# Performance work log

Measured on AMD Instinct MI355X. Metric: run time of the kernel, lower is better.

## Reference

```python
import jax, jax.numpy as jnp
import numpy as np

M, B, T, DIN, H, E, NEMB = 6, 128, 32, 64, 512, 512, 32


def setup_inputs() -> dict:
    key = jax.random.key(0)
    ks = jax.random.split(key, 6)
    return {
        "state_btD": jax.random.normal(ks[0], (B, T, M * DIN), dtype=jnp.float32),
        "emb_ids": jax.random.randint(ks[1], (B,), 0, NEMB),
        # stacked per-modality, per-embodiment adapter params (all modalities share dims)
        "W1": 0.02 * jax.random.normal(ks[2], (M, NEMB, DIN, H), dtype=jnp.float32),
        "b1": jnp.zeros((M, NEMB, H), dtype=jnp.float32),
        "W2": 0.02 * jax.random.normal(ks[3], (M, NEMB, H, E), dtype=jnp.float32),
        "b2": jnp.zeros((M, NEMB, E), dtype=jnp.float32),
        "type_embed": 0.02 * jax.random.normal(ks[4], (M, E), dtype=jnp.float32),
    }


def reference(state_btD, emb_ids, W1, b1, W2, b2, type_embed):
    Bb, Tt, _ = state_btD.shape
    # slices are contiguous equal-size chunks -> (B, T, M, DIN)
    x = state_btD.reshape(Bb, Tt, M, DIN)
    # layer1: per-sample gathered weights W1[:, emb_ids] -> (M, B, DIN, H)
    h = jax.nn.relu(
        jnp.einsum('btmi,mbih->btmh', x, W1[:, emb_ids])
        + b1[:, emb_ids].transpose(1, 0, 2)[:, None]  # (B,1,M,H)
    )
    # layer2 + type embed
    z = (
        jnp.einsum('btmh,mbho->btmo', h, W2[:, emb_ids])
        + b2[:, emb_ids].transpose(1, 0, 2)[:, None]
        + type_embed[None, None]  # (1,1,M,E)
    )
    # torch.cat(tokens, dim=1): modality-major along the token axis -> (B, M*T, E)
    return z.transpose(0, 2, 1, 3).reshape(Bb, M * Tt, E)
```

## Files before the change

kernel.cpp:

```cpp
#include <hip/hip_runtime.h>

#define MM   6
#define BB   128
#define TT   32
#define DIN  64
#define HH   512
#define EE   512
#define NEMB 32
#define XP   72
#define HP   520
#define TRS  36

typedef __attribute__((ext_vector_type(8))) short bf16x8;
typedef __attribute__((ext_vector_type(4))) float f32x4;

static __device__ __forceinline__ unsigned short f2bf(float f) {
    unsigned int u = __float_as_uint(f);
    u += 0x7FFFu + ((u >> 16) & 1u);
    return (unsigned short)(u >> 16);
}
static __device__ __forceinline__ float bf2f(unsigned short h) {
    return __uint_as_float(((unsigned int)h) << 16);
}

__global__ void order_k(const int* __restrict__ emb_ids, int* __restrict__ ent) {
    __shared__ int cnt_s[NEMB], psum_s[NEMB], slot_s[BB], id_s[BB];
    int t = threadIdx.x;
    if (t < NEMB) cnt_s[t] = 0;
    __syncthreads();
    if (t < BB) { int id = emb_ids[t]; id_s[t] = id; slot_s[t] = atomicAdd(&cnt_s[id], 1); }
    __syncthreads();
    if (t == 0) { int r = 0; for (int i = 0; i < NEMB; ++i) { psum_s[i] = r; r += cnt_s[i]; } }
    __syncthreads();
    if (t < BB) {
        int id = id_s[t], sl = slot_s[t], base = psum_s[id] * MM, c = cnt_s[id];
        for (int mm = 0; mm < MM; ++mm) ent[base + mm * c + sl] = (t << 3) | mm;
    }
}

__global__ __launch_bounds__(256, 2) void tok_mfma4(
    const float* __restrict__ state,
    const int*   __restrict__ ent,
    const float* __restrict__ W1,
    const float* __restrict__ b1,
    const float* __restrict__ W2,
    const float* __restrict__ b2,
    const float* __restrict__ te,
    const int*   __restrict__ emb_ids,
    float* __restrict__ out)
{
    __shared__ __align__(16) unsigned char regA[10240];
    __shared__ __align__(16) unsigned short h_hi[TT][HP];
    __shared__ __align__(16) unsigned short h_lo[TT][HP];

    const int bid = blockIdx.x;
    const int s   = (bid & 7) * 96 + (bid >> 3);
    const int e   = ent[s];
    const int b   = e >> 3;
    const int m   = e & 7;
    const int id  = emb_ids[b];

    const int tid  = threadIdx.x;
    const int lane = tid & 63;
    const int w    = tid >> 6;
    const int lr   = lane & 15;
    const int lg   = lane >> 4;

    const float* W1p = W1 + (size_t)(m * NEMB + id) * DIN * HH;
    const float* b1p = b1 + (size_t)(m * NEMB + id) * HH;
    const float* W2p = W2 + (size_t)(m * NEMB + id) * HH * EE;
    const float* b2p = b2 + (size_t)(m * NEMB + id) * EE;
    const float* tep = te + m * EE;
    const float* xg  = state + (size_t)b * TT * (MM * DIN) + m * DIN;

    unsigned short (*x_hi)[XP] = (unsigned short(*)[XP])regA;
    unsigned short (*x_lo)[XP] = (unsigned short(*)[XP])(regA + 4608);

    #pragma unroll
    for (int kq = 0; kq < 2; ++kq) {
        int f  = kq * 256 + tid;
        int t  = f >> 4;
        int i4 = f & 15;
        float4 v = *reinterpret_cast<const float4*>(xg + (size_t)t * (MM * DIN) + i4 * 4);
        ushort4 hi, lo;
        hi.x = f2bf(v.x); lo.x = f2bf(v.x - bf2f(hi.x));
        hi.y = f2bf(v.y); lo.y = f2bf(v.y - bf2f(hi.y));
        hi.z = f2bf(v.z); lo.z = f2bf(v.z - bf2f(hi.z));
        hi.w = f2bf(v.w); lo.w = f2bf(v.w - bf2f(hi.w));
        *reinterpret_cast<ushort4*>(&x_hi[t][i4 * 4]) = hi;
        *reinterpret_cast<ushort4*>(&x_lo[t][i4 * 4]) = lo;
    }
    __syncthreads();

    bf16x8 xa_h[2][2], xa_l[2][2];
    #pragma unroll
    for (int rt = 0; rt < 2; ++rt)
        #pragma unroll
        for (int kk = 0; kk < 2; ++kk) {
            xa_h[rt][kk] = *reinterpret_cast<const bf16x8*>(&x_hi[rt * 16 + lr][kk * 32 + lg * 8]);
            xa_l[rt][kk] = *reinterpret_cast<const bf16x8*>(&x_lo[rt * 16 + lr][kk * 32 + lg * 8]);
        }

    #pragma unroll
    for (int j = 0; j < 8; ++j) {
        const int n = w * 128 + j * 16 + lr;
        float bv = b1p[n];
        f32x4 a0 = {bv, bv, bv, bv};
        f32x4 a1 = {bv, bv, bv, bv};
        #pragma unroll
        for (int kk = 0; kk < 2; ++kk) {
            const float* wp = W1p + (size_t)(kk * 32 + lg * 8) * HH + n;
            bf16x8 bh, bl;
            #pragma unroll
            for (int i = 0; i < 8; ++i) {
                float wv = wp[(size_t)i * HH];
                unsigned short h_ = f2bf(wv);
                bh[i] = (short)h_;
                bl[i] = (short)f2bf(wv - bf2f(h_));
            }
            a0 = __builtin_amdgcn_mfma_f32_16x16x32_bf16(xa_h[0][kk], bh, a0, 0, 0, 0);
            a0 = __builtin_amdgcn_mfma_f32_16x16x32_bf16(xa_h[0][kk], bl, a0, 0, 0, 0);
            a0 = __builtin_amdgcn_mfma_f32_16x16x32_bf16(xa_l[0][kk], bh, a0, 0, 0, 0);
            a1 = __builtin_amdgcn_mfma_f32_16x16x32_bf16(xa_h[1][kk], bh, a1, 0, 0, 0);
            a1 = __builtin_amdgcn_mfma_f32_16x16x32_bf16(xa_h[1][kk], bl, a1, 0, 0, 0);
            a1 = __builtin_amdgcn_mfma_f32_16x16x32_bf16(xa_l[1][kk], bh, a1, 0, 0, 0);
        }
        #pragma unroll
        for (int r = 0; r < 4; ++r) {
            float h0 = fmaxf(a0[r], 0.0f);
            unsigned short hh0 = f2bf(h0);
            h_hi[lg * 4 + r][n] = hh0;
            h_lo[lg * 4 + r][n] = f2bf(h0 - bf2f(hh0));
            float h1 = fmaxf(a1[r], 0.0f);
            unsigned short hh1 = f2bf(h1);
            h_hi[16 + lg * 4 + r][n] = hh1;
            h_lo[16 + lg * 4 + r][n] = f2bf(h1 - bf2f(hh1));
        }
    }
    __syncthreads();

    float* bounce = (float*)(regA + w * 2304);
    const int wr = lane >> 2;
    const int wc = (lane & 3) * 4;

    float bias2[8];
    #pragma unroll
    for (int j = 0; j < 8; ++j) {
        int n = w * 128 + j * 16 + lr;
        bias2[j] = b2p[n] + tep[n];
    }
    f32x4 acc[2][8];
    #pragma unroll
    for (int rt = 0; rt < 2; ++rt)
        #pragma unroll
        for (int j = 0; j < 8; ++j) {
            f32x4 t0 = {bias2[j], bias2[j], bias2[j], bias2[j]};
            acc[rt][j] = t0;
        }

    const float* src0 = W2p + (size_t)wr * EE + (w * 128 + wc);
    float4 ra = *reinterpret_cast<const float4*>(src0);
    float4 rb = *reinterpret_cast<const float4*>(src0 + (size_t)16 * EE);

    for (int kk = 0; kk < 16; ++kk) {
        bf16x8 ah0 = *reinterpret_cast<const bf16x8*>(&h_hi[lr][kk * 32 + lg * 8]);
        bf16x8 al0 = *reinterpret_cast<const bf16x8*>(&h_lo[lr][kk * 32 + lg * 8]);
        bf16x8 ah1 = *reinterpret_cast<const bf16x8*>(&h_hi[16 + lr][kk * 32 + lg * 8]);
        bf16x8 al1 = *reinterpret_cast<const bf16x8*>(&h_lo[16 + lr][kk * 32 + lg * 8]);
        #pragma unroll
        for (int j = 0; j < 8; ++j) {
            asm volatile("" ::: "memory");
            bounce[(wc + 0) * TRS + wr] = ra.x;
            bounce[(wc + 1) * TRS + wr] = ra.y;
            bounce[(wc + 2) * TRS + wr] = ra.z;
            bounce[(wc + 3) * TRS + wr] = ra.w;
            bounce[(wc + 0) * TRS + 16 + wr] = rb.x;
            bounce[(wc + 1) * TRS + 16 + wr] = rb.y;
            bounce[(wc + 2) * TRS + 16 + wr] = rb.z;
            bounce[(wc + 3) * TRS + 16 + wr] = rb.w;
            int nkk = (j == 7) ? kk + 1 : kk;
            int nj  = (j == 7) ? 0 : j + 1;
            const float* nsrc = (nkk < 16)
                ? W2p + (size_t)(nkk * 32 + wr) * EE + (w * 128 + nj * 16 + wc)
                : src0;
            float4 na = *reinterpret_cast<const float4*>(nsrc);
            float4 nb = *reinterpret_cast<const float4*>(nsrc + (size_t)16 * EE);
            asm volatile("s_waitcnt lgkmcnt(0)" ::: "memory");
            float4 f0 = *reinterpret_cast<const float4*>(&bounce[lr * TRS + lg * 8]);
            float4 f1 = *reinterpret_cast<const float4*>(&bounce[lr * TRS + lg * 8 + 4]);
            bf16x8 bh, bl;
            {
                const float* fv0 = &f0.x;
                const float* fv1 = &f1.x;
                #pragma unroll
                for (int i = 0; i < 4; ++i) {
                    unsigned short hb = f2bf(fv0[i]);
                    bh[i] = (short)hb;
                    bl[i] = (short)f2bf(fv0[i] - bf2f(hb));
                }
                #pragma unroll
                for (int i = 0; i < 4; ++i) {
                    unsigned short hb = f2bf(fv1[i]);
                    bh[4 + i] = (short)hb;
                    bl[4 + i] = (short)f2bf(fv1[i] - bf2f(hb));
                }
            }
            acc[0][j] = __builtin_amdgcn_mfma_f32_16x16x32_bf16(ah0, bh, acc[0][j], 0, 0, 0);
            acc[0][j] = __builtin_amdgcn_mfma_f32_16x16x32_bf16(ah0, bl, acc[0][j], 0, 0, 0);
            acc[0][j] = __builtin_amdgcn_mfma_f32_16x16x32_bf16(al0, bh, acc[0][j], 0, 0, 0);
            acc[1][j] = __builtin_amdgcn_mfma_f32_16x16x32_bf16(ah1, bh, acc[1][j], 0, 0, 0);
            acc[1][j] = __builtin_amdgcn_mfma_f32_16x16x32_bf16(ah1, bl, acc[1][j], 0, 0, 0);
            acc[1][j] = __builtin_amdgcn_mfma_f32_16x16x32_bf16(al1, bh, acc[1][j], 0, 0, 0);
            ra = na; rb = nb;
        }
    }

    float* outp = out + ((size_t)(b * MM + m) * TT) * EE;
    #pragma unroll
    for (int rt = 0; rt < 2; ++rt)
        #pragma unroll
        for (int j = 0; j < 8; ++j) {
            int n = w * 128 + j * 16 + lr;
            #pragma unroll
            for (int r = 0; r < 4; ++r) {
                int row = rt * 16 + lg * 4 + r;
                outp[(size_t)row * EE + n] = acc[rt][j][r];
            }
        }
}

extern "C" void kernel_launch(void* const* d_in, const int* in_sizes, int n_in,
                              void* d_out, int out_size, void* d_ws, size_t ws_size,
                              hipStream_t stream) {
    const float* state   = (const float*)d_in[0];
    const int*   emb_ids = (const int*)d_in[1];
    const float* W1      = (const float*)d_in[2];
    const float* b1      = (const float*)d_in[3];
    const float* W2      = (const float*)d_in[4];
    const float* b2      = (const float*)d_in[5];
    const float* te      = (const float*)d_in[6];
    float*       out     = (float*)d_out;

    int* ent = (int*)d_ws;

    order_k<<<dim3(1), dim3(128), 0, stream>>>(emb_ids, ent);
    tok_mfma4<<<dim3(BB * MM), dim3(256), 0, stream>>>(
        state, ent, W1, b1, W2, b2, te, emb_ids, out);
}
```

Before: 415.6 us.

## Use 512-thread blocks, drop LDS bounce for W2, truncate low-part bf16

Doubles the block to 8 waves, each owning 64 output columns instead of 128, which halves the per-wave accumulators and is meant to raise occupancy and latency hiding. The W2 operand is now loaded directly as strided scalar loads, one column per lane, which removes the LDS transpose bounce and its waitcnt stalls but gives up coalesced float4 global loads. The low bf16 part of each hi/lo split is now truncated instead of rounded, saving ALU work at a small accuracy cost.

```diff
diff --git a/kernel.cpp b/kernel.cpp
--- a/kernel.cpp
+++ b/kernel.cpp
@@ -9,7 +9,6 @@
 #define NEMB 32
 #define XP   72
 #define HP   520
-#define TRS  36
 
 typedef __attribute__((ext_vector_type(8))) short bf16x8;
 typedef __attribute__((ext_vector_type(4))) float f32x4;
@@ -22,6 +21,9 @@
 static __device__ __forceinline__ float bf2f(unsigned short h) {
     return __uint_as_float(((unsigned int)h) << 16);
 }
+static __device__ __forceinline__ unsigned short f2bf_t(float f) {
+    return (unsigned short)(__float_as_uint(f) >> 16);
+}
 
 __global__ void order_k(const int* __restrict__ emb_ids, int* __restrict__ ent) {
     __shared__ int cnt_s[NEMB], psum_s[NEMB], slot_s[BB], id_s[BB];
@@ -38,7 +40,7 @@
     }
 }
 
-__global__ __launch_bounds__(256, 2) void tok_mfma4(
+__global__ __launch_bounds__(512, 4) void tok_mfma5(
     const float* __restrict__ state,
     const int*   __restrict__ ent,
     const float* __restrict__ W1,
@@ -49,7 +51,8 @@
     const int*   __restrict__ emb_ids,
     float* __restrict__ out)
 {
-    __shared__ __align__(16) unsigned char regA[10240];
+    __shared__ __align__(16) unsigned short x_hi[TT][XP];
+    __shared__ __align__(16) unsigned short x_lo[TT][XP];
     __shared__ __align__(16) unsigned short h_hi[TT][HP];
     __shared__ __align__(16) unsigned short h_lo[TT][HP];
 
@@ -73,20 +76,15 @@
     const float* tep = te + m * EE;
     const float* xg  = state + (size_t)b * TT * (MM * DIN) + m * DIN;
 
-    unsigned short (*x_hi)[XP] = (unsigned short(*)[XP])regA;
-    unsigned short (*x_lo)[XP] = (unsigned short(*)[XP])(regA + 4608);
-
-    #pragma unroll
-    for (int kq = 0; kq < 2; ++kq) {
-        int f  = kq * 256 + tid;
-        int t  = f >> 4;
-        int i4 = f & 15;
+    {
+        int t  = tid >> 4;
+        int i4 = tid & 15;
         float4 v = *reinterpret_cast<const float4*>(xg + (size_t)t * (MM * DIN) + i4 * 4);
         ushort4 hi, lo;
-        hi.x = f2bf(v.x); lo.x = f2bf(v.x - bf2f(hi.x));
-        hi.y = f2bf(v.y); lo.y = f2bf(v.y - bf2f(hi.y));
-        hi.z = f2bf(v.z); lo.z = f2bf(v.z - bf2f(hi.z));
-        hi.w = f2bf(v.w); lo.w = f2bf(v.w - bf2f(hi.w));
+        hi.x = f2bf(v.x); lo.x = f2bf_t(v.x - bf2f(hi.x));
+        hi.y = f2bf(v.y); lo.y = f2bf_t(v.y - bf2f(hi.y));
+        hi.z = f2bf(v.z); lo.z = f2bf_t(v.z - bf2f(hi.z));
+        hi.w = f2bf(v.w); lo.w = f2bf_t(v.w - bf2f(hi.w));
         *reinterpret_cast<ushort4*>(&x_hi[t][i4 * 4]) = hi;
         *reinterpret_cast<ushort4*>(&x_lo[t][i4 * 4]) = lo;
     }
@@ -102,8 +100,8 @@
         }
 
     #pragma unroll
-    for (int j = 0; j < 8; ++j) {
-        const int n = w * 128 + j * 16 + lr;
+    for (int j = 0; j < 4; ++j) {
+        const int n = w * 64 + j * 16 + lr;
         float bv = b1p[n];
         f32x4 a0 = {bv, bv, bv, bv};
         f32x4 a1 = {bv, bv, bv, bv};
@@ -116,7 +114,7 @@
                 float wv = wp[(size_t)i * HH];
                 unsigned short h_ = f2bf(wv);
                 bh[i] = (short)h_;
-                bl[i] = (short)f2bf(wv - bf2f(h_));
+                bl[i] = (short)f2bf_t(wv - bf2f(h_));
             }
             a0 = __builtin_amdgcn_mfma_f32_16x16x32_bf16(xa_h[0][kk], bh, a0, 0, 0, 0);
             a0 = __builtin_amdgcn_mfma_f32_16x16x32_bf16(xa_h[0][kk], bl, a0, 0, 0, 0);
@@ -130,37 +128,34 @@
             float h0 = fmaxf(a0[r], 0.0f);
             unsigned short hh0 = f2bf(h0);
             h_hi[lg * 4 + r][n] = hh0;
-            h_lo[lg * 4 + r][n] = f2bf(h0 - bf2f(hh0));
+            h_lo[lg * 4 + r][n] = f2bf_t(h0 - bf2f(hh0));
             float h1 = fmaxf(a1[r], 0.0f);
             unsigned short hh1 = f2bf(h1);
             h_hi[16 + lg * 4 + r][n] = hh1;
-            h_lo[16 + lg * 4 + r][n] = f2bf(h1 - bf2f(hh1));
-        }
-    }
-    __syncthreads();
-
-    float* bounce = (float*)(regA + w * 2304);
-    const int wr = lane >> 2;
-    const int wc = (lane & 3) * 4;
-
-    float bias2[8];
-    #pragma unroll
-    for (int j = 0; j < 8; ++j) {
-        int n = w * 128 + j * 16 + lr;
+            h_lo[16 + lg * 4 + r][n] = f2bf_t(h1 - bf2f(hh1));
+        }
+    }
+    __syncthreads();
+
+    float bias2[4];
+    #pragma unroll
+    for (int j = 0; j < 4; ++j) {
+        int n = w * 64 + j * 16 + lr;
         bias2[j] = b2p[n] + tep[n];
     }
-    f32x4 acc[2][8];
+    f32x4 acc[2][4];
     #pragma unroll
     for (int rt = 0; rt < 2; ++rt)
         #pragma unroll
-        for (int j = 0; j < 8; ++j) {
+        for (int j = 0; j < 4; ++j) {
             f32x4 t0 = {bias2[j], bias2[j], bias2[j], bias2[j]};
             acc[rt][j] = t0;
         }
 
-    const float* src0 = W2p + (size_t)wr * EE + (w * 128 + wc);
-    float4 ra = *reinterpret_cast<const float4*>(src0);
-    float4 rb = *reinterpret_cast<const float4*>(src0 + (size_t)16 * EE);
+    float cur[8];
+    #pragma unroll
+    for (int i = 0; i < 8; ++i)
+        cur[i] = W2p[(size_t)(lg * 8 + i) * EE + (w * 64 + lr)];
 
     for (int kk = 0; kk < 16; ++kk) {
         bf16x8 ah0 = *reinterpret_cast<const bf16x8*>(&h_hi[lr][kk * 32 + lg * 8]);
@@ -168,42 +163,24 @@
         bf16x8 ah1 = *reinterpret_cast<const bf16x8*>(&h_hi[16 + lr][kk * 32 + lg * 8]);
         bf16x8 al1 = *reinterpret_cast<const bf16x8*>(&h_lo[16 + lr][kk * 32 + lg * 8]);
         #pragma unroll
-        for (int j = 0; j < 8; ++j) {
-            asm volatile("" ::: "memory");
-            bounce[(wc + 0) * TRS + wr] = ra.x;
-            bounce[(wc + 1) * TRS + wr] = ra.y;
-            bounce[(wc + 2) * TRS + wr] = ra.z;
-            bounce[(wc + 3) * TRS + wr] = ra.w;
-            bounce[(wc + 0) * TRS + 16 + wr] = rb.x;
-            bounce[(wc + 1) * TRS + 16 + wr] = rb.y;
-            bounce[(wc + 2) * TRS + 16 + wr] = rb.z;
-            bounce[(wc + 3) * TRS + 16 + wr] = rb.w;
-            int nkk = (j == 7) ? kk + 1 : kk;
-            int nj  = (j == 7) ? 0 : j + 1;
-            const float* nsrc = (nkk < 16)
-                ? W2p + (size_t)(nkk * 32 + wr) * EE + (w * 128 + nj * 16 + wc)
-                : src0;
-            float4 na = *reinterpret_cast<const float4*>(nsrc);
-            float4 nb = *reinterpret_cast<const float4*>(nsrc + (size_t)16 * EE);
-            asm volatile("s_waitcnt lgkmcnt(0)" ::: "memory");
-            float4 f0 = *reinterpret_cast<const float4*>(&bounce[lr * TRS + lg * 8]);
-            float4 f1 = *reinterpret_cast<const float4*>(&bounce[lr * TRS + lg * 8 + 4]);
+        for (int j = 0; j < 4; ++j) {
+            int nkk = (j == 3) ? kk + 1 : kk;
+            int nj  = (j == 3) ? 0 : j + 1;
+            float nxt[8];
+            if (nkk < 16) {
+                const float* wp = W2p + (size_t)(nkk * 32 + lg * 8) * EE + (w * 64 + nj * 16 + lr);
+                #pragma unroll
+                for (int i = 0; i < 8; ++i) nxt[i] = wp[(size_t)i * EE];
+            } else {
+                #pragma unroll
+                for (int i = 0; i < 8; ++i) nxt[i] = 0.0f;
+            }
             bf16x8 bh, bl;
-            {
-                const float* fv0 = &f0.x;
-                const float* fv1 = &f1.x;
-                #pragma unroll
-                for (int i = 0; i < 4; ++i) {
-                    unsigned short hb = f2bf(fv0[i]);
-                    bh[i] = (short)hb;
-                    bl[i] = (short)f2bf(fv0[i] - bf2f(hb));
-                }
-                #pragma unroll
-                for (int i = 0; i < 4; ++i) {
-                    unsigned short hb = f2bf(fv1[i]);
-                    bh[4 + i] = (short)hb;
-                    bl[4 + i] = (short)f2bf(fv1[i] - bf2f(hb));
-                }
+            #pragma unroll
+            for (int i = 0; i < 8; ++i) {
+                unsigned short hb = f2bf(cur[i]);
+                bh[i] = (short)hb;
+                bl[i] = (short)f2bf_t(cur[i] - bf2f(hb));
             }
             acc[0][j] = __builtin_amdgcn_mfma_f32_16x16x32_bf16(ah0, bh, acc[0][j], 0, 0, 0);
             acc[0][j] = __builtin_amdgcn_mfma_f32_16x16x32_bf16(ah0, bl, acc[0][j], 0, 0, 0);
@@ -211,7 +188,8 @@
             acc[1][j] = __builtin_amdgcn_mfma_f32_16x16x32_bf16(ah1, bh, acc[1][j], 0, 0, 0);
             acc[1][j] = __builtin_amdgcn_mfma_f32_16x16x32_bf16(ah1, bl, acc[1][j], 0, 0, 0);
             acc[1][j] = __builtin_amdgcn_mfma_f32_16x16x32_bf16(al1, bh, acc[1][j], 0, 0, 0);
-            ra = na; rb = nb;
+            #pragma unroll
+            for (int i = 0; i < 8; ++i) cur[i] = nxt[i];
         }
     }
 
@@ -219,8 +197,8 @@
     #pragma unroll
     for (int rt = 0; rt < 2; ++rt)
         #pragma unroll
-        for (int j = 0; j < 8; ++j) {
-            int n = w * 128 + j * 16 + lr;
+        for (int j = 0; j < 4; ++j) {
+            int n = w * 64 + j * 16 + lr;
             #pragma unroll
             for (int r = 0; r < 4; ++r) {
                 int row = rt * 16 + lg * 4 + r;
@@ -244,6 +222,6 @@
     int* ent = (int*)d_ws;
 
     order_k<<<dim3(1), dim3(128), 0, stream>>>(emb_ids, ent);
-    tok_mfma4<<<dim3(BB * MM), dim3(256), 0, stream>>>(
+    tok_mfma5<<<dim3(BB * MM), dim3(512), 0, stream>>>(
         state, ent, W1, b1, W2, b2, te, emb_ids, out);
 }
```

Result: faster. 387.0 us (-6.9%).
